# Kernel tuning notes

Hardware: AMD Instinct MI355X
Metric: run time of the kernel (lower is better)

## Reference

```python
import jax, jax.numpy as jnp
import numpy as np

H = 64  # rnn_size == input_size

def setup_inputs() -> dict:
    key = jax.random.key(0)
    ks = jax.random.split(key, 6)
    vocab = 32000
    B, T = 4096, 128
    s = 1.0 / np.sqrt(H)
    return {
        "inst": jax.random.randint(ks[0], (B, T), 0, vocab, dtype=jnp.int64),
        "embed_w": jax.random.normal(ks[1], (vocab + 1, H), dtype=jnp.float32),
        "W_ih": jax.random.uniform(ks[2], (4 * H, H), dtype=jnp.float32, minval=-s, maxval=s),
        "W_hh": jax.random.uniform(ks[3], (4 * H, H), dtype=jnp.float32, minval=-s, maxval=s),
        "b_ih": jax.random.uniform(ks[4], (4 * H,), dtype=jnp.float32, minval=-s, maxval=s),
        "b_hh": jax.random.uniform(ks[5], (4 * H,), dtype=jnp.float32, minval=-s, maxval=s),
    }

def _lstm_scan(xs, W_ih, W_hh, b_ih, b_hh):
    # xs: [T, B, H]. PyTorch LSTMCell gate order: i, f, g, o.
    B = xs.shape[1]
    # Precompute input projections for all timesteps in one big GEMM.
    x_proj = jnp.einsum('tbh,gh->tbg', xs, W_ih) + b_ih + b_hh  # [T, B, 4H]

    def step(carry, xp):
        h, c = carry
        gates = xp + h @ W_hh.T  # [B, 4H]
        i, f, g, o = jnp.split(gates, 4, axis=-1)
        c = jax.nn.sigmoid(f) * c + jax.nn.sigmoid(i) * jnp.tanh(g)
        h = jax.nn.sigmoid(o) * jnp.tanh(c)
        return (h, c), None

    h0 = jnp.zeros((B, H), dtype=xs.dtype)
    c0 = jnp.zeros((B, H), dtype=xs.dtype)
    (h, c), _ = jax.lax.scan(step, (h0, c0), x_proj)
    return h

def reference(inst, embed_w, W_ih, W_hh, b_ih, b_hh):
    # inst: [B, T] int; embedding lookup for whole sequence at once.
    xs = embed_w[inst]                 # [B, T, H]
    xs = jnp.swapaxes(xs, 0, 1)        # [T, B, H] for scan over time
    return _lstm_scan(xs, W_ih, W_hh, b_ih, b_hh)  # final h: [B, H]
```

## Files before the change

kernel.cpp:

```cpp
#include <hip/hip_runtime.h>
#include <hip/hip_bf16.h>

#define H_DIM   64
#define T_STEPS 128
#define B_TOT   4096
#define BB      8
#define SK      72
#define NTHREADS 512
#define XBATCH  8

typedef _Float16 half8  __attribute__((ext_vector_type(8)));
typedef __attribute__((ext_vector_type(4))) float f32x4;

#if __has_builtin(__builtin_amdgcn_exp2f)
#define EXP2(x) __builtin_amdgcn_exp2f(x)
#else
#define EXP2(x) exp2f(x)
#endif

__device__ __forceinline__ float sigmoid2(float xp) {
    return __builtin_amdgcn_rcpf(1.0f + EXP2(-xp));
}
__device__ __forceinline__ float tanh2(float xp) {
    return fmaf(-2.0f, __builtin_amdgcn_rcpf(EXP2(xp) + 1.0f), 1.0f);
}

__device__ __forceinline__ float xor8_dpp(float v) {
    return __int_as_float(__builtin_amdgcn_mov_dpp(
        __float_as_int(v), 0x128 , 0xf, 0xf, false));
}

__global__ __launch_bounds__(NTHREADS, 4) void lstm_fused(
    const int* __restrict__ inst, const float* __restrict__ embed,
    const float* __restrict__ Wih, const float* __restrict__ Whh,
    const float* __restrict__ bih, const float* __restrict__ bhh,
    float* __restrict__ out)
{
    __shared__ __align__(16) _Float16 sX[2][16][SK];
    __shared__ __align__(16) _Float16 sH[2][16][SK];
    __shared__ int sInst[BB * T_STEPS];

    const int tid  = (int)threadIdx.x;
    const int w    = tid >> 6;
    const int l    = tid & 63;
    const int lrow = l & 15;
    const int lk   = l >> 4;
    const bool losd = (lrow < 8);
    const int col   = w * 8 + (lrow & 7);
    const int rstar = losd ? 0 : 1;
    const int mrow  = lk * 4 + rstar;
    const int br    = lk * 2 + rstar;
    const int b0    = (int)blockIdx.x * BB;

    const float L2E     = 1.4426950408889634f;
    const float TWO_L2E = 2.8853900817779268f;

    for (int i = tid; i < BB * T_STEPS; i += NTHREADS)
        sInst[i] = inst[b0 * T_STEPS + i];

    for (int i = tid; i < 2 * 16 * SK; i += NTHREADS) {
        ((_Float16*)sX)[i] = (_Float16)0.0f;
        ((_Float16*)sH)[i] = (_Float16)0.0f;
    }
    __syncthreads();

    half8 wf[2][4];
    float bias[2];
#pragma unroll
    for (int q = 0; q < 2; ++q) {
        const int gate = q * 2 + (lrow >> 3);
        const float ws = (gate == 2) ? TWO_L2E : L2E;
        const int gcol = gate * 64 + col;
        bias[q] = (bih[gcol] + bhh[gcol]) * ws;
#pragma unroll
        for (int kf = 0; kf < 4; ++kf) {
            const float* src = (kf < 2 ? Wih : Whh) + (long)gcol * H_DIM + (kf & 1) * 32 + lk * 8;
            half8 v;
#pragma unroll
            for (int jj = 0; jj < 8; ++jj) v[jj] = (_Float16)(src[jj] * ws);
            wf[q][kf] = v;
        }
    }

    const int xmw = (w >> 1) * 4 + (w & 1);
    {
        const int idx = sInst[w * T_STEPS + 0];
        sX[0][xmw][l] = (_Float16)embed[(long)idx * H_DIM + l];
    }

    float xbuf[XBATCH];
#pragma unroll
    for (int j = 0; j < XBATCH; ++j) {
        const int idx = sInst[w * T_STEPS + 1 + j];
        xbuf[j] = embed[(long)idx * H_DIM + l];
    }
    __syncthreads();

    float creg = 0.f, hreg = 0.f;

    for (int tb = 0; tb < T_STEPS; tb += XBATCH) {
#pragma unroll
        for (int j = 0; j < XBATCH; ++j) {
            const int t   = tb + j;
            const int buf = j & 1;
            const int ob  = buf ^ 1;
            const bool pf = (t + 1 < T_STEPS);

            const float xcur = xbuf[j];

            if (j == XBATCH - 1 && pf) {
#pragma unroll
                for (int jj = 0; jj < XBATCH; ++jj) {
                    const int tt = t + 2 + jj;
                    if (tt < T_STEPS) {
                        const int idx = sInst[w * T_STEPS + tt];
                        xbuf[jj] = embed[(long)idx * H_DIM + l];
                    }
                }
            }

            half8 a0 = *reinterpret_cast<const half8*>(&sX[buf][lrow][lk * 8]);
            half8 a1 = *reinterpret_cast<const half8*>(&sX[buf][lrow][32 + lk * 8]);
            half8 a2 = *reinterpret_cast<const half8*>(&sH[buf][lrow][lk * 8]);
            half8 a3 = *reinterpret_cast<const half8*>(&sH[buf][lrow][32 + lk * 8]);

            f32x4 acc[2];
#pragma unroll
            for (int q = 0; q < 2; ++q) {
                f32x4 a = {bias[q], bias[q], bias[q], bias[q]};
                a = __builtin_amdgcn_mfma_f32_16x16x32_f16(a0, wf[q][0], a, 0, 0, 0);
                a = __builtin_amdgcn_mfma_f32_16x16x32_f16(a1, wf[q][1], a, 0, 0, 0);
                a = __builtin_amdgcn_mfma_f32_16x16x32_f16(a2, wf[q][2], a, 0, 0, 0);
                a = __builtin_amdgcn_mfma_f32_16x16x32_f16(a3, wf[q][3], a, 0, 0, 0);
                acc[q] = a;
            }

            const float recv0 = xor8_dpp(losd ? acc[0][1] : acc[0][0]);
            const float recv1 = xor8_dpp(losd ? acc[1][1] : acc[1][0]);
            const float vi = losd ? acc[0][0] : recv0;
            const float vf = losd ? recv0     : acc[0][1];
            const float vg = losd ? acc[1][0] : recv1;
            const float vo = losd ? recv1     : acc[1][1];

            const float iv = sigmoid2(vi);
            const float fv = sigmoid2(vf);
            const float gv = tanh2(vg);
            const float ov = sigmoid2(vo);
            const float cs = fmaf(fv, creg, iv * (gv * TWO_L2E));
            creg = cs;
            hreg = ov * tanh2(cs);

            if (pf) {
                sH[ob][mrow][col] = (_Float16)hreg;
                sX[ob][xmw][l]    = (_Float16)xcur;
            }
            __syncthreads();
        }
    }

    out[(long)(b0 + br) * H_DIM + col] = hreg;
}

extern "C" void kernel_launch(void* const* d_in, const int* in_sizes, int n_in,
                              void* d_out, int out_size, void* d_ws, size_t ws_size,
                              hipStream_t stream) {
    const int*   inst  = (const int*)  d_in[0];
    const float* embed = (const float*)d_in[1];
    const float* Wih   = (const float*)d_in[2];
    const float* Whh   = (const float*)d_in[3];
    const float* bih   = (const float*)d_in[4];
    const float* bhh   = (const float*)d_in[5];
    float* out = (float*)d_out;

    lstm_fused<<<B_TOT / BB, NTHREADS, 0, stream>>>(inst, embed, Wih, Whh, bih, bhh, out);
}
```

Before: 80.96 us.

## Precompute next step's input-projection MFMAs off the recurrent critical path

The x·W_ih MFMAs for step t+1 are now computed during step t into a double-buffered accumulator, so each step's critical path only holds the two h·W_hh MFMAs. The embedding pipeline is shifted one step further ahead so sX is filled two steps in advance. __syncthreads is replaced by an explicit lgkmcnt wait plus s_barrier. This adds register pressure and more complicated buffer indexing, and the relaxed barrier could reorder global stores if the compiler relies on it.

Measured after the change: 81.51 us. No clear change (+0.7%).

```diff
diff --git a/kernel.cpp b/kernel.cpp
--- a/kernel.cpp
+++ b/kernel.cpp
@@ -17,12 +17,19 @@
 #else
 #define EXP2(x) exp2f(x)
 #endif
+#define RCP(x) __builtin_amdgcn_rcpf(x)
+
+#define BLOCK_SYNC() do {                                      \
+    asm volatile("s_waitcnt lgkmcnt(0)" ::: "memory");         \
+    __builtin_amdgcn_s_barrier();                              \
+    asm volatile("" ::: "memory");                             \
+} while (0)
 
 __device__ __forceinline__ float sigmoid2(float xp) {
-    return __builtin_amdgcn_rcpf(1.0f + EXP2(-xp));
+    return RCP(1.0f + EXP2(-xp));
 }
 __device__ __forceinline__ float tanh2(float xp) {
-    return fmaf(-2.0f, __builtin_amdgcn_rcpf(EXP2(xp) + 1.0f), 1.0f);
+    return fmaf(-2.0f, RCP(EXP2(xp) + 1.0f), 1.0f);
 }
 
 __device__ __forceinline__ float xor8_dpp(float v) {
@@ -84,17 +91,32 @@
 
     const int xmw = (w >> 1) * 4 + (w & 1);
     {
-        const int idx = sInst[w * T_STEPS + 0];
-        sX[0][xmw][l] = (_Float16)embed[(long)idx * H_DIM + l];
+        const int i0 = sInst[w * T_STEPS + 0];
+        sX[0][xmw][l] = (_Float16)embed[(long)i0 * H_DIM + l];
+        const int i1 = sInst[w * T_STEPS + 1];
+        sX[1][xmw][l] = (_Float16)embed[(long)i1 * H_DIM + l];
     }
 
     float xbuf[XBATCH];
 #pragma unroll
     for (int j = 0; j < XBATCH; ++j) {
-        const int idx = sInst[w * T_STEPS + 1 + j];
+        const int idx = sInst[w * T_STEPS + 2 + j];
         xbuf[j] = embed[(long)idx * H_DIM + l];
     }
     __syncthreads();
+
+    f32x4 xacc0[2], xacc1[2];
+    {
+        half8 ax0 = *reinterpret_cast<const half8*>(&sX[0][lrow][lk * 8]);
+        half8 ax1 = *reinterpret_cast<const half8*>(&sX[0][lrow][32 + lk * 8]);
+#pragma unroll
+        for (int q = 0; q < 2; ++q) {
+            f32x4 a = {bias[q], bias[q], bias[q], bias[q]};
+            a = __builtin_amdgcn_mfma_f32_16x16x32_f16(ax0, wf[q][0], a, 0, 0, 0);
+            a = __builtin_amdgcn_mfma_f32_16x16x32_f16(ax1, wf[q][1], a, 0, 0, 0);
+            xacc0[q] = a;
+        }
+    }
 
     float creg = 0.f, hreg = 0.f;
 
@@ -106,12 +128,13 @@
             const int ob  = buf ^ 1;
             const bool pf = (t + 1 < T_STEPS);
 
-            const float xcur = xbuf[j];
-
-            if (j == XBATCH - 1 && pf) {
+            half8 a2 = *reinterpret_cast<const half8*>(&sH[buf][lrow][lk * 8]);
+            half8 a3 = *reinterpret_cast<const half8*>(&sH[buf][lrow][32 + lk * 8]);
+
+            if (j == XBATCH - 1) {
 #pragma unroll
                 for (int jj = 0; jj < XBATCH; ++jj) {
-                    const int tt = t + 2 + jj;
+                    const int tt = t + 3 + jj;
                     if (tt < T_STEPS) {
                         const int idx = sInst[w * T_STEPS + tt];
                         xbuf[jj] = embed[(long)idx * H_DIM + l];
@@ -119,20 +142,25 @@
                 }
             }
 
-            half8 a0 = *reinterpret_cast<const half8*>(&sX[buf][lrow][lk * 8]);
-            half8 a1 = *reinterpret_cast<const half8*>(&sX[buf][lrow][32 + lk * 8]);
-            half8 a2 = *reinterpret_cast<const half8*>(&sH[buf][lrow][lk * 8]);
-            half8 a3 = *reinterpret_cast<const half8*>(&sH[buf][lrow][32 + lk * 8]);
-
             f32x4 acc[2];
 #pragma unroll
             for (int q = 0; q < 2; ++q) {
-                f32x4 a = {bias[q], bias[q], bias[q], bias[q]};
-                a = __builtin_amdgcn_mfma_f32_16x16x32_f16(a0, wf[q][0], a, 0, 0, 0);
-                a = __builtin_amdgcn_mfma_f32_16x16x32_f16(a1, wf[q][1], a, 0, 0, 0);
+                f32x4 a = (j & 1) ? xacc1[q] : xacc0[q];
                 a = __builtin_amdgcn_mfma_f32_16x16x32_f16(a2, wf[q][2], a, 0, 0, 0);
                 a = __builtin_amdgcn_mfma_f32_16x16x32_f16(a3, wf[q][3], a, 0, 0, 0);
                 acc[q] = a;
+            }
+
+            if (pf) {
+                half8 ax0 = *reinterpret_cast<const half8*>(&sX[ob][lrow][lk * 8]);
+                half8 ax1 = *reinterpret_cast<const half8*>(&sX[ob][lrow][32 + lk * 8]);
+#pragma unroll
+                for (int q = 0; q < 2; ++q) {
+                    f32x4 a = {bias[q], bias[q], bias[q], bias[q]};
+                    a = __builtin_amdgcn_mfma_f32_16x16x32_f16(ax0, wf[q][0], a, 0, 0, 0);
+                    a = __builtin_amdgcn_mfma_f32_16x16x32_f16(ax1, wf[q][1], a, 0, 0, 0);
+                    if (j & 1) xacc0[q] = a; else xacc1[q] = a;
+                }
             }
 
             const float recv0 = xor8_dpp(losd ? acc[0][1] : acc[0][0]);
@@ -150,11 +178,12 @@
             creg = cs;
             hreg = ov * tanh2(cs);
 
-            if (pf) {
+            if (pf)
                 sH[ob][mrow][col] = (_Float16)hreg;
-                sX[ob][xmw][l]    = (_Float16)xcur;
-            }
-            __syncthreads();
+            if (t + 2 < T_STEPS)
+                sX[buf][xmw][l] = (_Float16)xbuf[j];
+
+            BLOCK_SYNC();
         }
     }
 
```

## Make each wave own four batch rows with register-resident weights and no block barriers

Applied to the files above, without the earlier changes.

Each wavefront now processes four batch rows independently and keeps every gate's input and recurrent weights in registers, so 16 MFMA column tiles run per gate per step. Hidden state goes through a per-wave LDS buffer, which removes the block-wide __syncthreads on every timestep. Embedding rows are fetched as float4 vectors one step ahead and packed to fp16 with cvt_pkrtz. In exchange, the MFMA M dimension is padded by replicating 4 rows to 16, so matrix work per step roughly doubles. The large register footprint forces one wave per SIMD and risks spills.

Result: slower. 155.1 us (+91.5%).

```diff
diff --git a/kernel.cpp b/kernel.cpp
--- a/kernel.cpp
+++ b/kernel.cpp
@@ -4,12 +4,13 @@
 #define H_DIM   64
 #define T_STEPS 128
 #define B_TOT   4096
-#define BB      8
-#define SK      72
-#define NTHREADS 512
-#define XBATCH  8
+#define RPW     4
+#define RPB     16
+#define NTHREADS 256
+#define HST     66
 
 typedef _Float16 half8  __attribute__((ext_vector_type(8)));
+typedef __fp16   fp16x2 __attribute__((ext_vector_type(2)));
 typedef __attribute__((ext_vector_type(4))) float f32x4;
 
 #if __has_builtin(__builtin_amdgcn_exp2f)
@@ -17,148 +18,140 @@
 #else
 #define EXP2(x) exp2f(x)
 #endif
+#define RCP(x) __builtin_amdgcn_rcpf(x)
 
 __device__ __forceinline__ float sigmoid2(float xp) {
-    return __builtin_amdgcn_rcpf(1.0f + EXP2(-xp));
+    return RCP(1.0f + EXP2(-xp));
 }
 __device__ __forceinline__ float tanh2(float xp) {
-    return fmaf(-2.0f, __builtin_amdgcn_rcpf(EXP2(xp) + 1.0f), 1.0f);
+    return fmaf(-2.0f, RCP(EXP2(xp) + 1.0f), 1.0f);
 }
 
-__device__ __forceinline__ float xor8_dpp(float v) {
-    return __int_as_float(__builtin_amdgcn_mov_dpp(
-        __float_as_int(v), 0x128 , 0xf, 0xf, false));
+__device__ __forceinline__ half8 cvt8(const float* f) {
+    union { unsigned u[4]; half8 h; } r;
+#pragma unroll
+    for (int i = 0; i < 4; ++i) {
+        fp16x2 p = __builtin_amdgcn_cvt_pkrtz(f[2 * i], f[2 * i + 1]);
+        r.u[i] = __builtin_bit_cast(unsigned, p);
+    }
+    return r.h;
 }
 
-__global__ __launch_bounds__(NTHREADS, 4) void lstm_fused(
+__global__ __launch_bounds__(NTHREADS, 1) void lstm_fused(
     const int* __restrict__ inst, const float* __restrict__ embed,
     const float* __restrict__ Wih, const float* __restrict__ Whh,
     const float* __restrict__ bih, const float* __restrict__ bhh,
     float* __restrict__ out)
 {
-    __shared__ __align__(16) _Float16 sX[2][16][SK];
-    __shared__ __align__(16) _Float16 sH[2][16][SK];
-    __shared__ int sInst[BB * T_STEPS];
+    __shared__ int sInst[RPB * T_STEPS];
+    __shared__ __align__(16) _Float16 sH[4][RPW][HST];
 
     const int tid  = (int)threadIdx.x;
     const int w    = tid >> 6;
     const int l    = tid & 63;
     const int lrow = l & 15;
     const int lk   = l >> 4;
-    const bool losd = (lrow < 8);
-    const int col   = w * 8 + (lrow & 7);
-    const int rstar = losd ? 0 : 1;
-    const int mrow  = lk * 4 + rstar;
-    const int br    = lk * 2 + rstar;
-    const int b0    = (int)blockIdx.x * BB;
+    const int b0   = (int)blockIdx.x * RPB;
 
     const float L2E     = 1.4426950408889634f;
     const float TWO_L2E = 2.8853900817779268f;
 
-    for (int i = tid; i < BB * T_STEPS; i += NTHREADS)
+    for (int i = tid; i < RPB * T_STEPS; i += NTHREADS)
         sInst[i] = inst[b0 * T_STEPS + i];
 
-    for (int i = tid; i < 2 * 16 * SK; i += NTHREADS) {
-        ((_Float16*)sX)[i] = (_Float16)0.0f;
-        ((_Float16*)sH)[i] = (_Float16)0.0f;
-    }
+    for (int i = l; i < RPW * HST; i += 64)
+        ((_Float16*)sH[w])[i] = (_Float16)0.0f;
     __syncthreads();
 
-    half8 wf[2][4];
-    float bias[2];
+    half8 wf[4][4][4];
+    float bias[4][4];
 #pragma unroll
-    for (int q = 0; q < 2; ++q) {
-        const int gate = q * 2 + (lrow >> 3);
-        const float ws = (gate == 2) ? TWO_L2E : L2E;
-        const int gcol = gate * 64 + col;
-        bias[q] = (bih[gcol] + bhh[gcol]) * ws;
+    for (int g = 0; g < 4; ++g) {
+        const float ws = (g == 2) ? TWO_L2E : L2E;
 #pragma unroll
-        for (int kf = 0; kf < 4; ++kf) {
-            const float* src = (kf < 2 ? Wih : Whh) + (long)gcol * H_DIM + (kf & 1) * 32 + lk * 8;
-            half8 v;
+        for (int cg = 0; cg < 4; ++cg) {
+            const int gcol = g * 64 + cg * 16 + lrow;
+            bias[g][cg] = (bih[gcol] + bhh[gcol]) * ws;
 #pragma unroll
-            for (int jj = 0; jj < 8; ++jj) v[jj] = (_Float16)(src[jj] * ws);
-            wf[q][kf] = v;
+            for (int kf = 0; kf < 4; ++kf) {
+                const float* src = (kf < 2 ? Wih : Whh) + (long)gcol * H_DIM + (kf & 1) * 32 + lk * 8;
+                half8 v;
+#pragma unroll
+                for (int jj = 0; jj < 8; ++jj) v[jj] = (_Float16)(src[jj] * ws);
+                wf[g][cg][kf] = v;
+            }
         }
     }
 
-    const int xmw = (w >> 1) * 4 + (w & 1);
+    const int* myInst = &sInst[(w * RPW + (lrow >> 2)) * T_STEPS];
+
+    float xf[16];
+    half8 ax0, ax1;
     {
-        const int idx = sInst[w * T_STEPS + 0];
-        sX[0][xmw][l] = (_Float16)embed[(long)idx * H_DIM + l];
+        const float* e0 = embed + (long)myInst[0] * H_DIM + lk * 8;
+        *reinterpret_cast<float4*>(&xf[0])  = *reinterpret_cast<const float4*>(e0);
+        *reinterpret_cast<float4*>(&xf[4])  = *reinterpret_cast<const float4*>(e0 + 4);
+        *reinterpret_cast<float4*>(&xf[8])  = *reinterpret_cast<const float4*>(e0 + 32);
+        *reinterpret_cast<float4*>(&xf[12]) = *reinterpret_cast<const float4*>(e0 + 36);
+        ax0 = cvt8(&xf[0]);
+        ax1 = cvt8(&xf[8]);
+        const float* e1 = embed + (long)myInst[1] * H_DIM + lk * 8;
+        *reinterpret_cast<float4*>(&xf[0])  = *reinterpret_cast<const float4*>(e1);
+        *reinterpret_cast<float4*>(&xf[4])  = *reinterpret_cast<const float4*>(e1 + 4);
+        *reinterpret_cast<float4*>(&xf[8])  = *reinterpret_cast<const float4*>(e1 + 32);
+        *reinterpret_cast<float4*>(&xf[12]) = *reinterpret_cast<const float4*>(e1 + 36);
     }
 
-    float xbuf[XBATCH];
+    float c[4] = {0.f, 0.f, 0.f, 0.f};
+    float h[4] = {0.f, 0.f, 0.f, 0.f};
+
+#pragma unroll 1
+    for (int t = 0; t < T_STEPS; ++t) {
+        half8 ah0 = *reinterpret_cast<const half8*>(&sH[w][lrow >> 2][lk * 8]);
+        half8 ah1 = *reinterpret_cast<const half8*>(&sH[w][lrow >> 2][32 + lk * 8]);
+
 #pragma unroll
-    for (int j = 0; j < XBATCH; ++j) {
-        const int idx = sInst[w * T_STEPS + 1 + j];
-        xbuf[j] = embed[(long)idx * H_DIM + l];
-    }
-    __syncthreads();
+        for (int cg = 0; cg < 4; ++cg) {
+            float s[4];
+#pragma unroll
+            for (int g = 0; g < 4; ++g) {
+                f32x4 a = {bias[g][cg], bias[g][cg], bias[g][cg], bias[g][cg]};
+                a = __builtin_amdgcn_mfma_f32_16x16x32_f16(ax0, wf[g][cg][0], a, 0, 0, 0);
+                a = __builtin_amdgcn_mfma_f32_16x16x32_f16(ax1, wf[g][cg][1], a, 0, 0, 0);
+                a = __builtin_amdgcn_mfma_f32_16x16x32_f16(ah0, wf[g][cg][2], a, 0, 0, 0);
+                a = __builtin_amdgcn_mfma_f32_16x16x32_f16(ah1, wf[g][cg][3], a, 0, 0, 0);
+                s[g] = a[0];
+            }
+            const float iv = sigmoid2(s[0]);
+            const float fv = sigmoid2(s[1]);
+            const float gv = tanh2(s[2]);
+            const float ov = sigmoid2(s[3]);
+            const float cs = fmaf(fv, c[cg], iv * (gv * TWO_L2E));
+            c[cg] = cs;
+            h[cg] = ov * tanh2(cs);
 
-    float creg = 0.f, hreg = 0.f;
+            if (t + 1 < T_STEPS)
+                sH[w][lk][cg * 16 + lrow] = (_Float16)h[cg];
+        }
 
-    for (int tb = 0; tb < T_STEPS; tb += XBATCH) {
-#pragma unroll
-        for (int j = 0; j < XBATCH; ++j) {
-            const int t   = tb + j;
-            const int buf = j & 1;
-            const int ob  = buf ^ 1;
-            const bool pf = (t + 1 < T_STEPS);
+        if (t + 1 < T_STEPS) {
+            ax0 = cvt8(&xf[0]);
+            ax1 = cvt8(&xf[8]);
+        }
+        if (t + 2 < T_STEPS) {
+            const float* e = embed + (long)myInst[t + 2] * H_DIM + lk * 8;
+            *reinterpret_cast<float4*>(&xf[0])  = *reinterpret_cast<const float4*>(e);
+            *reinterpret_cast<float4*>(&xf[4])  = *reinterpret_cast<const float4*>(e + 4);
+            *reinterpret_cast<float4*>(&xf[8])  = *reinterpret_cast<const float4*>(e + 32);
+            *reinterpret_cast<float4*>(&xf[12]) = *reinterpret_cast<const float4*>(e + 36);
+        }
 
-            const float xcur = xbuf[j];
-
-            if (j == XBATCH - 1 && pf) {
-#pragma unroll
-                for (int jj = 0; jj < XBATCH; ++jj) {
-                    const int tt = t + 2 + jj;
-                    if (tt < T_STEPS) {
-                        const int idx = sInst[w * T_STEPS + tt];
-                        xbuf[jj] = embed[(long)idx * H_DIM + l];
-                    }
-                }
-            }
-
-            half8 a0 = *reinterpret_cast<const half8*>(&sX[buf][lrow][lk * 8]);
-            half8 a1 = *reinterpret_cast<const half8*>(&sX[buf][lrow][32 + lk * 8]);
-            half8 a2 = *reinterpret_cast<const half8*>(&sH[buf][lrow][lk * 8]);
-            half8 a3 = *reinterpret_cast<const half8*>(&sH[buf][lrow][32 + lk * 8]);
-
-            f32x4 acc[2];
-#pragma unroll
-            for (int q = 0; q < 2; ++q) {
-                f32x4 a = {bias[q], bias[q], bias[q], bias[q]};
-                a = __builtin_amdgcn_mfma_f32_16x16x32_f16(a0, wf[q][0], a, 0, 0, 0);
-                a = __builtin_amdgcn_mfma_f32_16x16x32_f16(a1, wf[q][1], a, 0, 0, 0);
-                a = __builtin_amdgcn_mfma_f32_16x16x32_f16(a2, wf[q][2], a, 0, 0, 0);
-                a = __builtin_amdgcn_mfma_f32_16x16x32_f16(a3, wf[q][3], a, 0, 0, 0);
-                acc[q] = a;
-            }
-
-            const float recv0 = xor8_dpp(losd ? acc[0][1] : acc[0][0]);
-            const float recv1 = xor8_dpp(losd ? acc[1][1] : acc[1][0]);
-            const float vi = losd ? acc[0][0] : recv0;
-            const float vf = losd ? recv0     : acc[0][1];
-            const float vg = losd ? acc[1][0] : recv1;
-            const float vo = losd ? recv1     : acc[1][1];
-
-            const float iv = sigmoid2(vi);
-            const float fv = sigmoid2(vf);
-            const float gv = tanh2(vg);
-            const float ov = sigmoid2(vo);
-            const float cs = fmaf(fv, creg, iv * (gv * TWO_L2E));
-            creg = cs;
-            hreg = ov * tanh2(cs);
-
-            if (pf) {
-                sH[ob][mrow][col] = (_Float16)hreg;
-                sX[ob][xmw][l]    = (_Float16)xcur;
-            }
-            __syncthreads();
-        }
+        asm volatile("" ::: "memory");
     }
 
-    out[(long)(b0 + br) * H_DIM + col] = hreg;
+#pragma unroll
+    for (int cg = 0; cg < 4; ++cg)
+        out[(long)(b0 + w * RPW + lk) * H_DIM + cg * 16 + lrow] = h[cg];
 }
 
 extern "C" void kernel_launch(void* const* d_in, const int* in_sizes, int n_in,
@@ -172,5 +165,5 @@
     const float* bhh   = (const float*)d_in[5];
     float* out = (float*)d_out;
 
-    lstm_fused<<<B_TOT / BB, NTHREADS, 0, stream>>>(inst, embed, Wih, Whh, bih, bhh, out);
+    lstm_fused<<<B_TOT / RPB, NTHREADS, 0, stream>>>(inst, embed, Wih, Whh, bih, bhh, out);
 }
```
